# Kernel optimization log

Hardware: AMD Instinct MI355X
Metric: run time of the kernel (lower is better)

## Reference

```python
import jax, jax.numpy as jnp
import numpy as np

# Module constants (from init_kwargs)
X_RANGE = (-10.0, 10.0)
Y_RANGE = (-10.0, 10.0)
N_X = 64
N_Y = 64
B = 16
N_CTX = 1024


def make_grid():
    # x counted forward, y counted backwards (image-row convention):
    # grid[k*N_X + j] = (xs[j], ys[k]) with ys from max to min.
    xs = jnp.linspace(X_RANGE[0], X_RANGE[1], N_X, dtype=jnp.float32)
    ys = jnp.linspace(Y_RANGE[1], Y_RANGE[0], N_Y, dtype=jnp.float32)
    gx, gy = jnp.meshgrid(xs, ys)          # each (N_Y, N_X)
    return jnp.stack([gx, gy], axis=-1).reshape(-1, 2)  # (G, 2)


def setup_inputs() -> dict:
    key = jax.random.key(0)
    k1, k2 = jax.random.split(key)
    X = jax.random.uniform(k1, (B, N_CTX, 2), dtype=jnp.float32,
                           minval=X_RANGE[0], maxval=X_RANGE[1])
    Y = jax.random.normal(k2, (B, N_CTX, 2), dtype=jnp.float32)
    log_l_scale = jnp.zeros((), dtype=jnp.float32)  # log(1.0)
    return {"X": X, "Y": Y, "log_l_scale": log_l_scale}


def reference(X, Y, log_l_scale):
    grid = make_grid()                                  # (G, 2)
    l = jnp.exp(log_l_scale)
    # squared distances via expansion to avoid a (B,G,n,2) intermediate
    g2 = jnp.sum(grid * grid, axis=-1)                  # (G,)
    x2 = jnp.sum(X * X, axis=-1)                        # (B, n)
    gx = jnp.einsum('gd,bnd->bgn', grid, X)             # (B, G, n)
    d2 = g2[None, :, None] + x2[:, None, :] - 2.0 * gx  # (B, G, n)
    Gram = jnp.exp(-0.5 * d2 / (l * l))                 # RBF kernel, B=1
    # expand Y with a leading ones (density) channel
    ones = jnp.ones(Y.shape[:2] + (1,), dtype=Y.dtype)
    EY = jnp.concatenate([ones, Y], axis=-1)            # (B, n, 3)
    FM = jnp.einsum('bgn,bnc->bgc', Gram, EY)           # (B, G, 3)
    dens = FM[..., 0:1]
    FM = jnp.concatenate([dens, FM[..., 1:] / dens], axis=-1)
    # (B, G, 3) -> (B, 3, N_Y, N_X)
    return FM.reshape(X.shape[0], N_Y, N_X, 3).transpose(0, 3, 1, 2)
```

## Files before the change

kernel.cpp:

```cpp
#include <hip/hip_runtime.h>
#include <hip/hip_bf16.h>
#include <math.h>


#define NB     16
#define NCTX   1024
#define NG     4096
#define NC     64
#define NSPLIT 16
#define GQ     4

__global__ __launch_bounds__(256)
void ee_partial(const float* __restrict__ X,
                const float* __restrict__ Y,
                const float* __restrict__ log_l_scale,
                float* __restrict__ ws) {
    const int blk = blockIdx.x;
    const int b   = blk >> 6;
    const int r   = blk & 63;
    const int gq  = r >> 4;
    const int nc  = r & 15;
    const int n0  = nc * NC;
    const int iy0 = gq * 16;

    const float step  = 20.0f / 63.0f;
    const float scale = -0.72134752044448170f * expf(-2.0f * log_l_scale[0]);

    __shared__ float  wx[NC][64];
    __shared__ float  wy[NC][16];
    __shared__ float2 sy[NC];

    const float2* Xb = (const float2*)(X + (size_t)b * NCTX * 2);
    const float2* Yb = (const float2*)(Y + (size_t)b * NCTX * 2);

    for (int idx = threadIdx.x; idx < NC * 64; idx += 256) {
        const int j = idx >> 6, i = idx & 63;
        const float dx = (-10.0f + step * (float)i) - Xb[n0 + j].x;
        wx[j][i] = exp2f(dx * dx * scale);
    }
    for (int idx = threadIdx.x; idx < NC * 16; idx += 256) {
        const int j = idx >> 4, q = idx & 15;
        const float dy = (10.0f - step * (float)(iy0 + q)) - Xb[n0 + j].y;
        wy[j][q] = exp2f(dy * dy * scale);
    }
    if (threadIdx.x < NC) sy[threadIdx.x] = Yb[n0 + threadIdx.x];
    __syncthreads();

    const int ixp = threadIdx.x & 31;
    const int iyp = threadIdx.x >> 5;
    float c00 = 0, c01 = 0, c02 = 0;
    float c10 = 0, c11 = 0, c12 = 0;
    float c20 = 0, c21 = 0, c22 = 0;
    float c30 = 0, c31 = 0, c32 = 0;

#pragma unroll 4
    for (int n = 0; n < NC; ++n) {
        const float2 wxv = *(const float2*)&wx[n][ixp * 2];
        const float2 wyv = *(const float2*)&wy[n][iyp * 2];
        const float2 yv  = sy[n];
        const float pA0 = wyv.x * yv.x, pA1 = wyv.x * yv.y;
        const float pB0 = wyv.y * yv.x, pB1 = wyv.y * yv.y;
        c00 = fmaf(wxv.x, wyv.x, c00); c01 = fmaf(wxv.x, pA0, c01); c02 = fmaf(wxv.x, pA1, c02);
        c10 = fmaf(wxv.y, wyv.x, c10); c11 = fmaf(wxv.y, pA0, c11); c12 = fmaf(wxv.y, pA1, c12);
        c20 = fmaf(wxv.x, wyv.y, c20); c21 = fmaf(wxv.x, pB0, c21); c22 = fmaf(wxv.x, pB1, c22);
        c30 = fmaf(wxv.y, wyv.y, c30); c31 = fmaf(wxv.y, pB0, c31); c32 = fmaf(wxv.y, pB1, c32);
    }

    float* base = ws + (((size_t)(b * NSPLIT + nc)) * 3) * NG;
    const int g0 = (iy0 + 2 * iyp) * 64 + 2 * ixp;
    *(float2*)&base[g0]           = make_float2(c00, c10);
    *(float2*)&base[g0 + 64]      = make_float2(c20, c30);
    *(float2*)&base[NG + g0]      = make_float2(c01, c11);
    *(float2*)&base[NG + g0 + 64] = make_float2(c21, c31);
    *(float2*)&base[2*NG + g0]      = make_float2(c02, c12);
    *(float2*)&base[2*NG + g0 + 64] = make_float2(c22, c32);
}

__global__ __launch_bounds__(256)
void ee_reduce(const float* __restrict__ ws, float* __restrict__ out) {
    const int t = blockIdx.x * 256 + threadIdx.x;
    const int b = t >> 12, g = t & 4095;
    const float* base = ws + (size_t)b * NSPLIT * 3 * NG;
    float a0 = 0, a1 = 0, a2 = 0;
#pragma unroll
    for (int nc = 0; nc < NSPLIT; ++nc) {
        const float* p = base + nc * 3 * NG;
        a0 += p[g];
        a1 += p[NG + g];
        a2 += p[2 * NG + g];
    }
    const float inv = 1.0f / a0;
    float* ob = out + (size_t)b * 3 * NG;
    ob[g]          = a0;
    ob[NG + g]     = a1 * inv;
    ob[2 * NG + g] = a2 * inv;
}

extern "C" void kernel_launch(void* const* d_in, const int* in_sizes, int n_in,
                              void* d_out, int out_size, void* d_ws, size_t ws_size,
                              hipStream_t stream) {
    const float* X    = (const float*)d_in[0];
    const float* Y    = (const float*)d_in[1];
    const float* logl = (const float*)d_in[2];
    float* out = (float*)d_out;
    float* ws  = (float*)d_ws;

    ee_partial<<<dim3(NB * GQ * NSPLIT), dim3(256), 0, stream>>>(X, Y, logl, ws);
    ee_reduce <<<dim3(NB * NG / 256),    dim3(256), 0, stream>>>(ws, out);
}
```

Before: 72.90 us.

## Compute full 64x64 grid per block with 4x4 register tiles

Each block now covers the whole 64x64 grid for one (batch, context-chunk) pair instead of one 16-row quarter. Each thread accumulates a 4x4 tile per channel instead of 2x2, and the x/y exponential weights are computed once per block rather than the y part separately per quarter. The aim is to cut redundant exp work and shared-memory loads per FMA. In exchange the grid shrinks from 1024 to 256 blocks, close to one per CU on a 256-CU part, and each thread holds 48 accumulators, so latency hiding and occupancy may suffer.

```diff
diff --git a/kernel.cpp b/kernel.cpp
--- a/kernel.cpp
+++ b/kernel.cpp
@@ -6,28 +6,23 @@
 #define NB     16
 #define NCTX   1024
 #define NG     4096
+#define NSPLIT 16
 #define NC     64
-#define NSPLIT 16
-#define GQ     4
 
-__global__ __launch_bounds__(256)
+__global__ __launch_bounds__(256, 1)
 void ee_partial(const float* __restrict__ X,
                 const float* __restrict__ Y,
                 const float* __restrict__ log_l_scale,
                 float* __restrict__ ws) {
-    const int blk = blockIdx.x;
-    const int b   = blk >> 6;
-    const int r   = blk & 63;
-    const int gq  = r >> 4;
-    const int nc  = r & 15;
-    const int n0  = nc * NC;
-    const int iy0 = gq * 16;
+    const int b  = blockIdx.x >> 4;
+    const int nc = blockIdx.x & 15;
+    const int n0 = nc * NC;
 
     const float step  = 20.0f / 63.0f;
     const float scale = -0.72134752044448170f * expf(-2.0f * log_l_scale[0]);
 
     __shared__ float  wx[NC][64];
-    __shared__ float  wy[NC][16];
+    __shared__ float  wy[NC][64];
     __shared__ float2 sy[NC];
 
     const float2* Xb = (const float2*)(X + (size_t)b * NCTX * 2);
@@ -35,45 +30,52 @@
 
     for (int idx = threadIdx.x; idx < NC * 64; idx += 256) {
         const int j = idx >> 6, i = idx & 63;
-        const float dx = (-10.0f + step * (float)i) - Xb[n0 + j].x;
+        const float2 xv = Xb[n0 + j];
+        const float dx = (-10.0f + step * (float)i) - xv.x;
+        const float dy = ( 10.0f - step * (float)i) - xv.y;
         wx[j][i] = exp2f(dx * dx * scale);
-    }
-    for (int idx = threadIdx.x; idx < NC * 16; idx += 256) {
-        const int j = idx >> 4, q = idx & 15;
-        const float dy = (10.0f - step * (float)(iy0 + q)) - Xb[n0 + j].y;
-        wy[j][q] = exp2f(dy * dy * scale);
+        wy[j][i] = exp2f(dy * dy * scale);
     }
     if (threadIdx.x < NC) sy[threadIdx.x] = Yb[n0 + threadIdx.x];
     __syncthreads();
 
-    const int ixp = threadIdx.x & 31;
-    const int iyp = threadIdx.x >> 5;
-    float c00 = 0, c01 = 0, c02 = 0;
-    float c10 = 0, c11 = 0, c12 = 0;
-    float c20 = 0, c21 = 0, c22 = 0;
-    float c30 = 0, c31 = 0, c32 = 0;
+    const int tx = threadIdx.x & 15;
+    const int ty = threadIdx.x >> 4;
+    const int ix0 = tx * 4;
+    const int iy0 = ty * 4;
+
+    float4 ad[4] = {{0,0,0,0},{0,0,0,0},{0,0,0,0},{0,0,0,0}};
+    float4 a1[4] = {{0,0,0,0},{0,0,0,0},{0,0,0,0},{0,0,0,0}};
+    float4 a2[4] = {{0,0,0,0},{0,0,0,0},{0,0,0,0},{0,0,0,0}};
 
 #pragma unroll 4
     for (int n = 0; n < NC; ++n) {
-        const float2 wxv = *(const float2*)&wx[n][ixp * 2];
-        const float2 wyv = *(const float2*)&wy[n][iyp * 2];
+        const float4 wxv = *(const float4*)&wx[n][ix0];
+        const float4 wyv = *(const float4*)&wy[n][iy0];
         const float2 yv  = sy[n];
-        const float pA0 = wyv.x * yv.x, pA1 = wyv.x * yv.y;
-        const float pB0 = wyv.y * yv.x, pB1 = wyv.y * yv.y;
-        c00 = fmaf(wxv.x, wyv.x, c00); c01 = fmaf(wxv.x, pA0, c01); c02 = fmaf(wxv.x, pA1, c02);
-        c10 = fmaf(wxv.y, wyv.x, c10); c11 = fmaf(wxv.y, pA0, c11); c12 = fmaf(wxv.y, pA1, c12);
-        c20 = fmaf(wxv.x, wyv.y, c20); c21 = fmaf(wxv.x, pB0, c21); c22 = fmaf(wxv.x, pB1, c22);
-        c30 = fmaf(wxv.y, wyv.y, c30); c31 = fmaf(wxv.y, pB0, c31); c32 = fmaf(wxv.y, pB1, c32);
+        const float wys[4] = {wyv.x, wyv.y, wyv.z, wyv.w};
+#pragma unroll
+        for (int s = 0; s < 4; ++s) {
+            const float w  = wys[s];
+            const float q1 = w * yv.x;
+            const float q2 = w * yv.y;
+            ad[s].x = fmaf(wxv.x, w, ad[s].x);  ad[s].y = fmaf(wxv.y, w, ad[s].y);
+            ad[s].z = fmaf(wxv.z, w, ad[s].z);  ad[s].w = fmaf(wxv.w, w, ad[s].w);
+            a1[s].x = fmaf(wxv.x, q1, a1[s].x); a1[s].y = fmaf(wxv.y, q1, a1[s].y);
+            a1[s].z = fmaf(wxv.z, q1, a1[s].z); a1[s].w = fmaf(wxv.w, q1, a1[s].w);
+            a2[s].x = fmaf(wxv.x, q2, a2[s].x); a2[s].y = fmaf(wxv.y, q2, a2[s].y);
+            a2[s].z = fmaf(wxv.z, q2, a2[s].z); a2[s].w = fmaf(wxv.w, q2, a2[s].w);
+        }
     }
 
-    float* base = ws + (((size_t)(b * NSPLIT + nc)) * 3) * NG;
-    const int g0 = (iy0 + 2 * iyp) * 64 + 2 * ixp;
-    *(float2*)&base[g0]           = make_float2(c00, c10);
-    *(float2*)&base[g0 + 64]      = make_float2(c20, c30);
-    *(float2*)&base[NG + g0]      = make_float2(c01, c11);
-    *(float2*)&base[NG + g0 + 64] = make_float2(c21, c31);
-    *(float2*)&base[2*NG + g0]      = make_float2(c02, c12);
-    *(float2*)&base[2*NG + g0 + 64] = make_float2(c22, c32);
+    float* base = ws + ((size_t)(b * NSPLIT + nc)) * 3 * NG;
+#pragma unroll
+    for (int s = 0; s < 4; ++s) {
+        const int g = (iy0 + s) * 64 + ix0;
+        *(float4*)&base[g]          = ad[s];
+        *(float4*)&base[NG + g]     = a1[s];
+        *(float4*)&base[2*NG + g]   = a2[s];
+    }
 }
 
 __global__ __launch_bounds__(256)
@@ -105,6 +107,6 @@
     float* out = (float*)d_out;
     float* ws  = (float*)d_ws;
 
-    ee_partial<<<dim3(NB * GQ * NSPLIT), dim3(256), 0, stream>>>(X, Y, logl, ws);
-    ee_reduce <<<dim3(NB * NG / 256),    dim3(256), 0, stream>>>(ws, out);
+    ee_partial<<<dim3(NB * NSPLIT), dim3(256), 0, stream>>>(X, Y, logl, ws);
+    ee_reduce <<<dim3(NB * NG / 256), dim3(256), 0, stream>>>(ws, out);
 }
```

After: 72.54 us. About the same (-0.5%).
